# Kernel tuning notes

Measured on AMD Instinct MI355X. Metric: run time of the kernel, lower is better.

The kernel has to match this reference:

```python
import jax, jax.numpy as jnp
import numpy as np

B, S, D = 4, 2048, 1024
NUM_HEADS = 16
KQ = D // NUM_HEADS  # 64


def setup_inputs() -> dict:
    key = jax.random.key(0)
    ks = jax.random.split(key, 4)
    # he_uniform fan_in = D: limit = sqrt(6/fan_in)
    lim = np.sqrt(6.0 / D).astype(np.float32)
    x = jax.random.normal(ks[0], (B, S, D), dtype=jnp.float32)
    Wq = jax.random.uniform(ks[1], (D, KQ), minval=-lim, maxval=lim, dtype=jnp.float32)
    Wk = jax.random.uniform(ks[2], (D, KQ), minval=-lim, maxval=lim, dtype=jnp.float32)
    Wv = jax.random.uniform(ks[3], (D, KQ), minval=-lim, maxval=lim, dtype=jnp.float32)
    Bq = jnp.zeros((S, KQ), dtype=jnp.float32)
    Bk = jnp.zeros((S, KQ), dtype=jnp.float32)
    Bv = jnp.zeros((S, KQ), dtype=jnp.float32)
    return {"x": x, "Wq": Wq, "Bq": Bq, "Wk": Wk, "Bk": Bk, "Wv": Wv, "Bv": Bv}


def reference(x, Wq, Bq, Wk, Bk, Wv, Bv):
    # Q/K/V: [B,S,KQ]; biases are per-position [S,KQ], broadcast over batch
    Q = jnp.einsum('bsd,dk->bsk', x, Wq) + Bq
    K = jnp.einsum('bsd,dk->bsk', x, Wk) + Bk
    V = jnp.einsum('bsd,dk->bsk', x, Wv) + Bv
    scale = 1.0 / jnp.sqrt(jnp.float32(KQ))
    scores = jnp.einsum('bqk,bsk->bqs', Q, K) * scale  # [B,S,S]
    attn = jax.nn.softmax(scores, axis=-1)
    return jnp.einsum('bqs,bsk->bqk', attn, V)  # [B,S,KQ]
```

## Files before the change

kernel.cpp:

```cpp
#include <hip/hip_runtime.h>
#include <stdint.h>

#define NBATCH 4
#define NS 2048
#define ND 1024
#define NK 64
#define QSCALE 0.18033688011112042f

typedef __attribute__((ext_vector_type(4))) float f32x4;
typedef __attribute__((ext_vector_type(16))) float f32x16;
typedef __attribute__((ext_vector_type(8))) short bf16x8;
typedef unsigned short u16;
typedef unsigned int u32;
typedef unsigned long long u64;

__device__ __forceinline__ u16 f2bf(float f) {
  union { float f; u32 u; } v; v.f = f;
  u32 u = v.u;
  u += 0x7FFFu + ((u >> 16) & 1u);
  return (u16)(u >> 16);
}

__device__ __forceinline__ u32 pk2(float lo, float hi) {
  u32 r;
  asm("v_cvt_pk_bf16_f32 %0, %1, %2" : "=v"(r) : "v"(lo), "v"(hi));
  return r;
}

__global__ __launch_bounds__(256) void wtrans_kernel(
    const float* __restrict__ Wq, const float* __restrict__ Wk,
    const float* __restrict__ Wv, u16* __restrict__ Wt) {
  __shared__ float tile[64][65];
  int blk = blockIdx.x;
  int m = blk >> 4, dt = blk & 15;
  const float* W = (m == 0) ? Wq : (m == 1) ? Wk : Wv;
  int d0 = dt * 64;
  int t = threadIdx.x;
#pragma unroll
  for (int i = 0; i < 16; i++) {
    int idx = t + 256 * i;
    int dd = idx >> 6, c = idx & 63;
    tile[dd][c] = W[(d0 + dd) * 64 + c];
  }
  __syncthreads();
#pragma unroll
  for (int i = 0; i < 16; i++) {
    int idx = t + 256 * i;
    int c = idx >> 6, dd = idx & 63;
    Wt[(m * 64 + c) * 1024 + d0 + dd] = f2bf(tile[dd][c]);
  }
}

__global__ __launch_bounds__(512) void qkv_kernel(
    const float* __restrict__ x, const u16* __restrict__ Wt,
    const float* __restrict__ Bq, const float* __restrict__ Bk,
    const float* __restrict__ Bv, u16* __restrict__ Qf,
    u16* __restrict__ Kf, u16* __restrict__ Vf) {
  __shared__ __attribute__((aligned(16))) char lds[57344];
  char* ldsx = lds;
  char* ldsw = lds + 8192;

  int tid = threadIdx.x;
  int w = tid >> 6, lane = tid & 63;
  int g = lane >> 4, c = lane & 15;
  int rh = w & 1, cq = w >> 1;

  int xrow = tid >> 4;
  int xp4  = tid & 15;
  const float* xsrc = x + ((long)blockIdx.x * 32 + xrow) * ND + xp4 * 4;
  int xwoff = xrow * 128 + ((xp4 * 8) ^ ((xrow & 7) << 4));

  int wrow = tid >> 3;
  int wslot = tid & 7;
  const u16* wsrc0 = Wt + (long)wrow * ND + wslot * 8;
  const u16* wsrc1 = Wt + (long)(64 + wrow) * ND + wslot * 8;
  const u16* wsrc2 = Wt + (long)(128 + wrow) * ND + wslot * 8;
  int wswz = (wrow & 7) << 4;
  int wwoff0 = wrow * 128 + ((wslot * 16) ^ wswz);
  int wwoff1 = (64 + wrow) * 128 + ((wslot * 16) ^ wswz);
  int wwoff2 = (128 + wrow) * 128 + ((wslot * 16) ^ wswz);

  int rowa = rh * 16 + c;
  int aswz = (rowa & 7) << 4;
  int aoff0 = rowa * 128 + ((g * 16) ^ aswz);
  int aoff1 = rowa * 128 + ((64 + g * 16) ^ aswz);
  int boff00, boff01, boff10, boff11, boff20, boff21;
  {
    int col = cq * 48 + c;
    int bz = (col & 7) << 4;
    boff00 = col * 128 + ((g * 16) ^ bz);
    boff01 = col * 128 + ((64 + g * 16) ^ bz);
    col += 16; bz = (col & 7) << 4;
    boff10 = col * 128 + ((g * 16) ^ bz);
    boff11 = col * 128 + ((64 + g * 16) ^ bz);
    col += 16; bz = (col & 7) << 4;
    boff20 = col * 128 + ((g * 16) ^ bz);
    boff21 = col * 128 + ((64 + g * 16) ^ bz);
  }

  f32x4 acc[3];
#pragma unroll
  for (int tt = 0; tt < 3; tt++) acc[tt] = (f32x4){0.f, 0.f, 0.f, 0.f};

  f32x4 xst;
  bf16x8 wst0, wst1, wst2;

#define LOADS(T) do {                                   \
    xst  = *(const f32x4*)(xsrc + (T) * 64);            \
    wst0 = *(const bf16x8*)(wsrc0 + (T) * 64);          \
    wst1 = *(const bf16x8*)(wsrc1 + (T) * 64);          \
    wst2 = *(const bf16x8*)(wsrc2 + (T) * 64);          \
  } while (0)

#define WRITES(NB) do {                                 \
    u32 lo_ = pk2(xst[0], xst[1]);                      \
    u32 hi_ = pk2(xst[2], xst[3]);                      \
    *(u64*)(ldsx + (NB) * 4096 + xwoff) = ((u64)hi_ << 32) | lo_; \
    *(bf16x8*)(ldsw + (NB) * 24576 + wwoff0) = wst0;    \
    *(bf16x8*)(ldsw + (NB) * 24576 + wwoff1) = wst1;    \
    *(bf16x8*)(ldsw + (NB) * 24576 + wwoff2) = wst2;    \
  } while (0)

#define COMPUTE(B) do {                                 \
    const char* xb_ = ldsx + (B) * 4096;                \
    const char* wb_ = ldsw + (B) * 24576;               \
    bf16x8 a0_ = *(const bf16x8*)(xb_ + aoff0);         \
    bf16x8 a1_ = *(const bf16x8*)(xb_ + aoff1);         \
    acc[0] = __builtin_amdgcn_mfma_f32_16x16x32_bf16(a0_, *(const bf16x8*)(wb_ + boff00), acc[0], 0, 0, 0); \
    acc[0] = __builtin_amdgcn_mfma_f32_16x16x32_bf16(a1_, *(const bf16x8*)(wb_ + boff01), acc[0], 0, 0, 0); \
    acc[1] = __builtin_amdgcn_mfma_f32_16x16x32_bf16(a0_, *(const bf16x8*)(wb_ + boff10), acc[1], 0, 0, 0); \
    acc[1] = __builtin_amdgcn_mfma_f32_16x16x32_bf16(a1_, *(const bf16x8*)(wb_ + boff11), acc[1], 0, 0, 0); \
    acc[2] = __builtin_amdgcn_mfma_f32_16x16x32_bf16(a0_, *(const bf16x8*)(wb_ + boff20), acc[2], 0, 0, 0); \
    acc[2] = __builtin_amdgcn_mfma_f32_16x16x32_bf16(a1_, *(const bf16x8*)(wb_ + boff21), acc[2], 0, 0, 0); \
  } while (0)

  LOADS(0);
  WRITES(0);
  __syncthreads();
#pragma unroll
  for (int t = 0; t < 16; t++) {
    if (t < 15) LOADS(t + 1);
    __builtin_amdgcn_sched_barrier(0);
    COMPUTE(t & 1);
    if (t < 15) WRITES((t + 1) & 1);
    __syncthreads();
  }
#undef LOADS
#undef WRITES
#undef COMPUTE

  long r0 = (long)blockIdx.x * 32 + rh * 16 + 4 * g;
#pragma unroll
  for (int tt = 0; tt < 3; tt++) {
    int colg = cq * 48 + tt * 16 + c;
    int mtx = colg >> 6;
    int col = colg & 63;
    const float* Bias = (mtx == 0) ? Bq : (mtx == 1) ? Bk : Bv;
    u16* Out = (mtx == 0) ? Qf : (mtx == 1) ? Kf : Vf;
#pragma unroll
    for (int j = 0; j < 4; j++) {
      long r = r0 + j;
      int srow = (int)(r & (NS - 1));
      int bb = (int)(r >> 11);
      float v = acc[tt][j] + Bias[srow * NK + col];
      if (mtx == 0) v *= QSCALE;
      long addr;
      if (mtx < 2) {
        addr = (((long)bb * 64 + (srow >> 5)) * 4 + (col >> 4)) * 512
             + (long)((srow & 31) + ((col >> 3) & 1) * 32) * 8 + (col & 7);
      } else {
        addr = ((((long)bb * 2 + ((col >> 5) & 1)) * 32 + (srow >> 6)) * 4 + ((srow >> 4) & 3)) * 512
             + (long)((col & 31) + ((srow >> 3) & 1) * 32) * 8 + (srow & 7);
      }
      Out[addr] = f2bf(v);
    }
  }
}

__device__ __forceinline__ bf16x8 pack8(float p0, float p1, float p2, float p3,
                                        float p4, float p5, float p6, float p7,
                                        int hi) {
  u32 A = pk2(p0, p1), B = pk2(p2, p3), C = pk2(p4, p5), D = pk2(p6, p7);
  u32 sA = (u32)__shfl_xor((int)A, 32);
  u32 sB = (u32)__shfl_xor((int)B, 32);
  u32 sC = (u32)__shfl_xor((int)C, 32);
  u32 sD = (u32)__shfl_xor((int)D, 32);
  union { u32 w[4]; bf16x8 v; } u;
  u.w[0] = hi ? sC : A;
  u.w[1] = hi ? sD : B;
  u.w[2] = hi ? C : sA;
  u.w[3] = hi ? D : sB;
  return u.v;
}

__global__ __launch_bounds__(512) void attn_kernel(
    const u16* __restrict__ Qf, const u16* __restrict__ Kf,
    const u16* __restrict__ Vf, float* __restrict__ out) {
  __shared__ float Ol[8][32][64];
  __shared__ float Ll[8][32];
  int w = threadIdx.x >> 6, lane = threadIdx.x & 63;
  int q = lane & 31, hi = lane >> 5;
  int bid = blockIdx.x;
  int b = (bid & 7) >> 1;
  int qt = ((bid >> 3) << 1) | (bid & 1);
  long qglob = (long)b * NS + qt * 32;

  bf16x8 qf[4];
  {
    const u16* qp = Qf + ((long)b * 64 + qt) * 2048 + lane * 8;
#pragma unroll
    for (int kk = 0; kk < 4; kk++) qf[kk] = *(const bf16x8*)(qp + kk * 512);
  }
  const u16* kcp = Kf + ((long)b * 64 + w * 8) * 2048 + lane * 8;
  const u16* vcp0 = Vf + ((long)b * 64 + w * 4) * 2048 + lane * 8;
  const u16* vcp1 = Vf + ((long)(b * 2 + 1) * 32 + w * 4) * 2048 + lane * 8;

  f32x16 o0, o1;
#pragma unroll
  for (int r = 0; r < 16; r++) { o0[r] = 0.f; o1[r] = 0.f; }
  float lacc[4] = {0.f, 0.f, 0.f, 0.f};

  bf16x8 kA0[4], kA1[4], kB0[4], kB1[4];
#pragma unroll
  for (int kk = 0; kk < 4; kk++) {
    kA0[kk] = *(const bf16x8*)(kcp + kk * 512);
    kA1[kk] = *(const bf16x8*)(kcp + 2048 + kk * 512);
  }

#define ATTN_STEP(T, KC0, KC1, KN0, KN1)                                      \
  do {                                                                        \
    int t_ = (T);                                                             \
    bf16x8 vf0[4], vf1[4];                                                    \
    _Pragma("unroll") for (int i = 0; i < 4; i++) {                           \
      vf0[i] = *(const bf16x8*)(vcp0 + t_ * 2048 + i * 512);                  \
      vf1[i] = *(const bf16x8*)(vcp1 + t_ * 2048 + i * 512);                  \
    }                                                                         \
    if (t_ + 1 < 4) {                                                         \
      const u16* kn_ = kcp + (long)(t_ + 1) * 4096;                           \
      _Pragma("unroll") for (int i = 0; i < 4; i++) {                         \
        KN0[i] = *(const bf16x8*)(kn_ + i * 512);                             \
        KN1[i] = *(const bf16x8*)(kn_ + 2048 + i * 512);                      \
      }                                                                       \
    }                                                                         \
    __builtin_amdgcn_sched_barrier(0);                                        \
    f32x16 s0, s1;                                                            \
    _Pragma("unroll") for (int r = 0; r < 16; r++) { s0[r] = 0.f; s1[r] = 0.f; } \
    _Pragma("unroll") for (int i = 0; i < 4; i++)                             \
      s0 = __builtin_amdgcn_mfma_f32_32x32x16_bf16(KC0[i], qf[i], s0, 0, 0, 0); \
    _Pragma("unroll") for (int i = 0; i < 4; i++)                             \
      s1 = __builtin_amdgcn_mfma_f32_32x32x16_bf16(KC1[i], qf[i], s1, 0, 0, 0); \
    _Pragma("unroll") for (int r = 0; r < 16; r++) {                          \
      s0[r] = exp2f(s0[r]); s1[r] = exp2f(s1[r]);                             \
      lacc[r & 3] += s0[r] + s1[r];                                           \
    }                                                                         \
    bf16x8 pa[4];                                                             \
    pa[0] = pack8(s0[0], s0[1], s0[2], s0[3], s0[4], s0[5], s0[6], s0[7], hi);   \
    pa[1] = pack8(s0[8], s0[9], s0[10], s0[11], s0[12], s0[13], s0[14], s0[15], hi); \
    pa[2] = pack8(s1[0], s1[1], s1[2], s1[3], s1[4], s1[5], s1[6], s1[7], hi);   \
    pa[3] = pack8(s1[8], s1[9], s1[10], s1[11], s1[12], s1[13], s1[14], s1[15], hi); \
    _Pragma("unroll") for (int i = 0; i < 4; i++) {                           \
      o0 = __builtin_amdgcn_mfma_f32_32x32x16_bf16(pa[i], vf0[i], o0, 0, 0, 0); \
      o1 = __builtin_amdgcn_mfma_f32_32x32x16_bf16(pa[i], vf1[i], o1, 0, 0, 0); \
    }                                                                         \
  } while (0)

  ATTN_STEP(0, kA0, kA1, kB0, kB1);
  ATTN_STEP(1, kB0, kB1, kA0, kA1);
  ATTN_STEP(2, kA0, kA1, kB0, kB1);
  ATTN_STEP(3, kB0, kB1, kA0, kA1);
#undef ATTN_STEP

  float lt = (lacc[0] + lacc[1]) + (lacc[2] + lacc[3]);
  lt += __shfl_xor(lt, 32);

#pragma unroll
  for (int r = 0; r < 16; r++) {
    int qq = (r & 3) + 8 * (r >> 2) + 4 * hi;
    Ol[w][qq][q]      = o0[r];
    Ol[w][qq][q + 32] = o1[r];
  }
  if (hi == 0) Ll[w][q] = lt;
  __syncthreads();

#pragma unroll
  for (int rr = 4; rr >= 1; rr >>= 1) {
    if (w < rr) {
#pragma unroll
      for (int i = 0; i < 8; i++) {
        int idx = lane + i * 64;
        f32x4* dst = (f32x4*)&Ol[w][idx >> 4][(idx & 15) * 4];
        const f32x4* src = (const f32x4*)&Ol[w + rr][idx >> 4][(idx & 15) * 4];
        *dst += *src;
      }
      if (lane < 32) Ll[w][lane] += Ll[w + rr][lane];
    }
    __syncthreads();
  }

  {
    int idx = threadIdx.x;
    int row = idx >> 4, c4 = (idx & 15) * 4;
    float inv = 1.0f / Ll[0][row];
    f32x4 v = *(const f32x4*)&Ol[0][row][c4];
    f32x4 r;
#pragma unroll
    for (int i = 0; i < 4; i++) r[i] = v[i] * inv;
    *(f32x4*)&out[(qglob + row) * NK + c4] = r;
  }
}

extern "C" void kernel_launch(void* const* d_in, const int* in_sizes, int n_in,
                              void* d_out, int out_size, void* d_ws, size_t ws_size,
                              hipStream_t stream) {
  const float* x  = (const float*)d_in[0];
  const float* Wq = (const float*)d_in[1];
  const float* Bq = (const float*)d_in[2];
  const float* Wk = (const float*)d_in[3];
  const float* Bk = (const float*)d_in[4];
  const float* Wv = (const float*)d_in[5];
  const float* Bv = (const float*)d_in[6];
  float* out = (float*)d_out;

  char* ws = (char*)d_ws;
  u16* Wt = (u16*)ws;
  u16* Qf = (u16*)(ws + 393216);
  u16* Kf = (u16*)(ws + 1441792);
  u16* Vf = (u16*)(ws + 2490368);

  wtrans_kernel<<<dim3(48), dim3(256), 0, stream>>>(Wq, Wk, Wv, Wt);
  qkv_kernel<<<dim3(256), dim3(512), 0, stream>>>(x, Wt, Bq, Bk, Bv, Qf, Kf, Vf);
  attn_kernel<<<dim3(256), dim3(512), 0, stream>>>(Qf, Kf, Vf, out);
}
```

Measured before the change: 34.19 us.

## Share K/V tiles across waves via double-buffered LDS and split keys across blocks

```diff
diff --git a/kernel.cpp b/kernel.cpp
--- a/kernel.cpp
+++ b/kernel.cpp
@@ -193,62 +193,71 @@
   return u.v;
 }
 
-__global__ __launch_bounds__(512) void attn_kernel(
+__global__ __launch_bounds__(256) void attn_kernel(
     const u16* __restrict__ Qf, const u16* __restrict__ Kf,
-    const u16* __restrict__ Vf, float* __restrict__ out) {
-  __shared__ float Ol[8][32][64];
-  __shared__ float Ll[8][32];
-  int w = threadIdx.x >> 6, lane = threadIdx.x & 63;
+    const u16* __restrict__ Vf, float* __restrict__ Opart,
+    float* __restrict__ lpart) {
+  __shared__ __attribute__((aligned(16))) char kv[2][16384];
+  int tid = threadIdx.x;
+  int w = tid >> 6, lane = tid & 63;
   int q = lane & 31, hi = lane >> 5;
   int bid = blockIdx.x;
-  int b = (bid & 7) >> 1;
-  int qt = ((bid >> 3) << 1) | (bid & 1);
-  long qglob = (long)b * NS + qt * 32;
+  int xcd = bid & 7, i5 = bid >> 3;
+  int combo = xcd * 2 + (i5 & 1);
+  int qt4 = i5 >> 1;
+  int b = combo >> 2, sp = combo & 3;
 
   bf16x8 qf[4];
   {
-    const u16* qp = Qf + ((long)b * 64 + qt) * 2048 + lane * 8;
+    const u16* qp = Qf + ((long)b * 64 + qt4 * 4 + w) * 2048 + lane * 8;
 #pragma unroll
     for (int kk = 0; kk < 4; kk++) qf[kk] = *(const bf16x8*)(qp + kk * 512);
   }
-  const u16* kcp = Kf + ((long)b * 64 + w * 8) * 2048 + lane * 8;
-  const u16* vcp0 = Vf + ((long)b * 64 + w * 4) * 2048 + lane * 8;
-  const u16* vcp1 = Vf + ((long)(b * 2 + 1) * 32 + w * 4) * 2048 + lane * 8;
+
+  const char* ksrc = (const char*)(Kf + ((long)b * 64 + sp * 16) * 2048);
+  const char* v0src = (const char*)(Vf + ((long)(b * 2) * 32 + sp * 8) * 2048);
+  const char* v1src = (const char*)(Vf + ((long)(b * 2 + 1) * 32 + sp * 8) * 2048);
+  const char* src_base = (w == 0) ? ksrc : (w == 1) ? (ksrc + 4096)
+                       : (w == 2) ? v0src : v1src;
+  long src_step = (w < 2) ? 8192 : 4096;
+  int ldsoff = w * 4096 + lane * 16;
 
   f32x16 o0, o1;
 #pragma unroll
   for (int r = 0; r < 16; r++) { o0[r] = 0.f; o1[r] = 0.f; }
   float lacc[4] = {0.f, 0.f, 0.f, 0.f};
 
-  bf16x8 kA0[4], kA1[4], kB0[4], kB1[4];
-#pragma unroll
-  for (int kk = 0; kk < 4; kk++) {
-    kA0[kk] = *(const bf16x8*)(kcp + kk * 512);
-    kA1[kk] = *(const bf16x8*)(kcp + 2048 + kk * 512);
-  }
-
-#define ATTN_STEP(T, KC0, KC1, KN0, KN1)                                      \
-  do {                                                                        \
-    int t_ = (T);                                                             \
-    bf16x8 vf0[4], vf1[4];                                                    \
+  bf16x8 g0, g1, g2, g3;
+#define SLOAD(T) do {                                                   \
+    const char* s_ = src_base + (long)(T) * src_step + lane * 16;       \
+    g0 = *(const bf16x8*)(s_);                                          \
+    g1 = *(const bf16x8*)(s_ + 1024);                                   \
+    g2 = *(const bf16x8*)(s_ + 2048);                                   \
+    g3 = *(const bf16x8*)(s_ + 3072);                                   \
+  } while (0)
+#define SWRITE(NB) do {                                                 \
+    char* d_ = kv[NB] + ldsoff;                                         \
+    *(bf16x8*)(d_)        = g0;                                         \
+    *(bf16x8*)(d_ + 1024) = g1;                                         \
+    *(bf16x8*)(d_ + 2048) = g2;                                         \
+    *(bf16x8*)(d_ + 3072) = g3;                                         \
+  } while (0)
+
+#define ASTEP(T) do {                                                         \
+    const char* base_ = kv[(T) & 1];                                          \
+    bf16x8 kf0[4], kf1[4], vf0[4], vf1[4];                                    \
     _Pragma("unroll") for (int i = 0; i < 4; i++) {                           \
-      vf0[i] = *(const bf16x8*)(vcp0 + t_ * 2048 + i * 512);                  \
-      vf1[i] = *(const bf16x8*)(vcp1 + t_ * 2048 + i * 512);                  \
+      kf0[i] = *(const bf16x8*)(base_ + i * 1024 + lane * 16);                \
+      kf1[i] = *(const bf16x8*)(base_ + 4096 + i * 1024 + lane * 16);         \
+      vf0[i] = *(const bf16x8*)(base_ + 8192 + i * 1024 + lane * 16);         \
+      vf1[i] = *(const bf16x8*)(base_ + 12288 + i * 1024 + lane * 16);        \
     }                                                                         \
-    if (t_ + 1 < 4) {                                                         \
-      const u16* kn_ = kcp + (long)(t_ + 1) * 4096;                           \
-      _Pragma("unroll") for (int i = 0; i < 4; i++) {                         \
-        KN0[i] = *(const bf16x8*)(kn_ + i * 512);                             \
-        KN1[i] = *(const bf16x8*)(kn_ + 2048 + i * 512);                      \
-      }                                                                       \
-    }                                                                         \
-    __builtin_amdgcn_sched_barrier(0);                                        \
     f32x16 s0, s1;                                                            \
     _Pragma("unroll") for (int r = 0; r < 16; r++) { s0[r] = 0.f; s1[r] = 0.f; } \
     _Pragma("unroll") for (int i = 0; i < 4; i++)                             \
-      s0 = __builtin_amdgcn_mfma_f32_32x32x16_bf16(KC0[i], qf[i], s0, 0, 0, 0); \
+      s0 = __builtin_amdgcn_mfma_f32_32x32x16_bf16(kf0[i], qf[i], s0, 0, 0, 0); \
     _Pragma("unroll") for (int i = 0; i < 4; i++)                             \
-      s1 = __builtin_amdgcn_mfma_f32_32x32x16_bf16(KC1[i], qf[i], s1, 0, 0, 0); \
+      s1 = __builtin_amdgcn_mfma_f32_32x32x16_bf16(kf1[i], qf[i], s1, 0, 0, 0); \
     _Pragma("unroll") for (int r = 0; r < 16; r++) {                          \
       s0[r] = exp2f(s0[r]); s1[r] = exp2f(s1[r]);                             \
       lacc[r & 3] += s0[r] + s1[r];                                           \
@@ -264,49 +273,51 @@
     }                                                                         \
   } while (0)
 
-  ATTN_STEP(0, kA0, kA1, kB0, kB1);
-  ATTN_STEP(1, kB0, kB1, kA0, kA1);
-  ATTN_STEP(2, kA0, kA1, kB0, kB1);
-  ATTN_STEP(3, kB0, kB1, kA0, kA1);
-#undef ATTN_STEP
+  SLOAD(0);
+  SWRITE(0);
+  __syncthreads();
+#pragma unroll
+  for (int t = 0; t < 8; t++) {
+    if (t < 7) SLOAD(t + 1);
+    ASTEP(t);
+    if (t < 7) SWRITE((t + 1) & 1);
+    __syncthreads();
+  }
+#undef SLOAD
+#undef SWRITE
+#undef ASTEP
 
   float lt = (lacc[0] + lacc[1]) + (lacc[2] + lacc[3]);
   lt += __shfl_xor(lt, 32);
 
+  long qbase = (long)b * NS + (qt4 * 4 + w) * 32;
+  long ob = (long)sp * (NBATCH * NS * NK);
 #pragma unroll
   for (int r = 0; r < 16; r++) {
     int qq = (r & 3) + 8 * (r >> 2) + 4 * hi;
-    Ol[w][qq][q]      = o0[r];
-    Ol[w][qq][q + 32] = o1[r];
-  }
-  if (hi == 0) Ll[w][q] = lt;
-  __syncthreads();
-
-#pragma unroll
-  for (int rr = 4; rr >= 1; rr >>= 1) {
-    if (w < rr) {
-#pragma unroll
-      for (int i = 0; i < 8; i++) {
-        int idx = lane + i * 64;
-        f32x4* dst = (f32x4*)&Ol[w][idx >> 4][(idx & 15) * 4];
-        const f32x4* src = (const f32x4*)&Ol[w + rr][idx >> 4][(idx & 15) * 4];
-        *dst += *src;
-      }
-      if (lane < 32) Ll[w][lane] += Ll[w + rr][lane];
-    }
-    __syncthreads();
-  }
-
-  {
-    int idx = threadIdx.x;
-    int row = idx >> 4, c4 = (idx & 15) * 4;
-    float inv = 1.0f / Ll[0][row];
-    f32x4 v = *(const f32x4*)&Ol[0][row][c4];
-    f32x4 r;
-#pragma unroll
-    for (int i = 0; i < 4; i++) r[i] = v[i] * inv;
-    *(f32x4*)&out[(qglob + row) * NK + c4] = r;
-  }
+    float* op = Opart + ob + (qbase + qq) * NK + q;
+    op[0]  = o0[r];
+    op[32] = o1[r];
+  }
+  if (hi == 0) lpart[sp * (NBATCH * NS) + qbase + q] = lt;
+}
+
+__global__ __launch_bounds__(256) void combine_kernel(
+    const float* __restrict__ Opart, const float* __restrict__ lpart,
+    float* __restrict__ out, int nsplit) {
+  int gid = blockIdx.x * 256 + threadIdx.x;
+  int rw = gid >> 4, c4 = (gid & 15) * 4;
+  f32x4 a = (f32x4){0.f, 0.f, 0.f, 0.f};
+  float l = 0.f;
+  for (int sp = 0; sp < nsplit; sp++) {
+    a += *(const f32x4*)(Opart + (long)sp * (NBATCH * NS * NK) + (long)rw * NK + c4);
+    l += lpart[sp * (NBATCH * NS) + rw];
+  }
+  float inv = 1.0f / l;
+  f32x4 r;
+#pragma unroll
+  for (int i = 0; i < 4; i++) r[i] = a[i] * inv;
+  *(f32x4*)(out + (long)rw * NK + c4) = r;
 }
 
 extern "C" void kernel_launch(void* const* d_in, const int* in_sizes, int n_in,
@@ -326,8 +337,11 @@
   u16* Qf = (u16*)(ws + 393216);
   u16* Kf = (u16*)(ws + 1441792);
   u16* Vf = (u16*)(ws + 2490368);
+  float* lpart = (float*)(ws + 3538944);
+  float* Opart = (float*)(ws + 3801088);
 
   wtrans_kernel<<<dim3(48), dim3(256), 0, stream>>>(Wq, Wk, Wv, Wt);
   qkv_kernel<<<dim3(256), dim3(512), 0, stream>>>(x, Wt, Bq, Bk, Bv, Qf, Kf, Vf);
-  attn_kernel<<<dim3(256), dim3(512), 0, stream>>>(Qf, Kf, Vf, out);
-}
+  attn_kernel<<<dim3(256), dim3(256), 0, stream>>>(Qf, Kf, Vf, Opart, lpart);
+  combine_kernel<<<dim3(512), dim3(256), 0, stream>>>(Opart, lpart, out, 4);
+}
```

Result: slower. 40.18 us (+17.5%).

## Use direct global-to-LDS loads with triple buffering and staged epilogue stores in QKV

Applied to the files above, without the earlier changes.

```diff
diff --git a/kernel.cpp b/kernel.cpp
--- a/kernel.cpp
+++ b/kernel.cpp
@@ -25,6 +25,12 @@
   u32 r;
   asm("v_cvt_pk_bf16_f32 %0, %1, %2" : "=v"(r) : "v"(lo), "v"(hi));
   return r;
+}
+
+__device__ __forceinline__ void gll16(const void* g, void* l) {
+  __builtin_amdgcn_global_load_lds(
+      (const __attribute__((address_space(1))) unsigned int*)g,
+      (__attribute__((address_space(3))) unsigned int*)l, 16, 0, 0);
 }
 
 __global__ __launch_bounds__(256) void wtrans_kernel(
@@ -56,124 +62,125 @@
     const float* __restrict__ Bq, const float* __restrict__ Bk,
     const float* __restrict__ Bv, u16* __restrict__ Qf,
     u16* __restrict__ Kf, u16* __restrict__ Vf) {
-  __shared__ __attribute__((aligned(16))) char lds[57344];
+  __shared__ __attribute__((aligned(16))) char lds[98304];
   char* ldsx = lds;
-  char* ldsw = lds + 8192;
+  char* ldsw = lds + 24576;
 
   int tid = threadIdx.x;
   int w = tid >> 6, lane = tid & 63;
   int g = lane >> 4, c = lane & 15;
   int rh = w & 1, cq = w >> 1;
 
-  int xrow = tid >> 4;
-  int xp4  = tid & 15;
-  const float* xsrc = x + ((long)blockIdx.x * 32 + xrow) * ND + xp4 * 4;
-  int xwoff = xrow * 128 + ((xp4 * 8) ^ ((xrow & 7) << 4));
-
-  int wrow = tid >> 3;
-  int wslot = tid & 7;
-  const u16* wsrc0 = Wt + (long)wrow * ND + wslot * 8;
-  const u16* wsrc1 = Wt + (long)(64 + wrow) * ND + wslot * 8;
-  const u16* wsrc2 = Wt + (long)(128 + wrow) * ND + wslot * 8;
-  int wswz = (wrow & 7) << 4;
-  int wwoff0 = wrow * 128 + ((wslot * 16) ^ wswz);
-  int wwoff1 = (64 + wrow) * 128 + ((wslot * 16) ^ wswz);
-  int wwoff2 = (128 + wrow) * 128 + ((wslot * 16) ^ wswz);
+  int xrow_l = 4 * w + (lane >> 4);
+  long xrow_g = (long)blockIdx.x * 32 + xrow_l;
+  int xs32 = ((lane >> 1) & 7) ^ (xrow_l & 7);
+  const char* xg = (const char*)(x + xrow_g * ND) + xs32 * 32 + (lane & 1) * 16;
+
+  int wr0 = 8 * w + (lane >> 3);
+  const char* wg0 = (const char*)(Wt + (long)(wr0)       * ND) + (((lane & 7) ^ (wr0 & 7)) * 16);
+  const char* wg1 = (const char*)(Wt + (long)(64 + wr0)  * ND) + (((lane & 7) ^ (wr0 & 7)) * 16);
+  const char* wg2 = (const char*)(Wt + (long)(128 + wr0) * ND) + (((lane & 7) ^ (wr0 & 7)) * 16);
+  int wd0 = (8 * w) * 128, wd1 = (64 + 8 * w) * 128, wd2 = (128 + 8 * w) * 128;
 
   int rowa = rh * 16 + c;
-  int aswz = (rowa & 7) << 4;
-  int aoff0 = rowa * 128 + ((g * 16) ^ aswz);
-  int aoff1 = rowa * 128 + ((64 + g * 16) ^ aswz);
-  int boff00, boff01, boff10, boff11, boff20, boff21;
-  {
-    int col = cq * 48 + c;
-    int bz = (col & 7) << 4;
-    boff00 = col * 128 + ((g * 16) ^ bz);
-    boff01 = col * 128 + ((64 + g * 16) ^ bz);
-    col += 16; bz = (col & 7) << 4;
-    boff10 = col * 128 + ((g * 16) ^ bz);
-    boff11 = col * 128 + ((64 + g * 16) ^ bz);
-    col += 16; bz = (col & 7) << 4;
-    boff20 = col * 128 + ((g * 16) ^ bz);
-    boff21 = col * 128 + ((64 + g * 16) ^ bz);
+  int axor = rowa & 7;
+  int aoff0 = rowa * 256 + ((g ^ axor) * 32);
+  int aoff1 = rowa * 256 + (((4 + g) ^ axor) * 32);
+  int boff[3][2];
+#pragma unroll
+  for (int tt = 0; tt < 3; tt++) {
+    int col = cq * 48 + tt * 16 + c;
+#pragma unroll
+    for (int kk = 0; kk < 2; kk++)
+      boff[tt][kk] = col * 128 + (((kk * 4 + g) ^ (col & 7)) * 16);
   }
 
   f32x4 acc[3];
 #pragma unroll
   for (int tt = 0; tt < 3; tt++) acc[tt] = (f32x4){0.f, 0.f, 0.f, 0.f};
 
-  f32x4 xst;
-  bf16x8 wst0, wst1, wst2;
-
-#define LOADS(T) do {                                   \
-    xst  = *(const f32x4*)(xsrc + (T) * 64);            \
-    wst0 = *(const bf16x8*)(wsrc0 + (T) * 64);          \
-    wst1 = *(const bf16x8*)(wsrc1 + (T) * 64);          \
-    wst2 = *(const bf16x8*)(wsrc2 + (T) * 64);          \
+#define STAGE(BUF, T) do {                                            \
+    gll16(xg + (long)(T) * 256, ldsx + (BUF) * 8192 + w * 1024);      \
+    gll16(wg0 + (T) * 128, ldsw + (BUF) * 24576 + wd0);               \
+    gll16(wg1 + (T) * 128, ldsw + (BUF) * 24576 + wd1);               \
+    gll16(wg2 + (T) * 128, ldsw + (BUF) * 24576 + wd2);               \
   } while (0)
 
-#define WRITES(NB) do {                                 \
-    u32 lo_ = pk2(xst[0], xst[1]);                      \
-    u32 hi_ = pk2(xst[2], xst[3]);                      \
-    *(u64*)(ldsx + (NB) * 4096 + xwoff) = ((u64)hi_ << 32) | lo_; \
-    *(bf16x8*)(ldsw + (NB) * 24576 + wwoff0) = wst0;    \
-    *(bf16x8*)(ldsw + (NB) * 24576 + wwoff1) = wst1;    \
-    *(bf16x8*)(ldsw + (NB) * 24576 + wwoff2) = wst2;    \
+#define COMPUTE(B) do {                                               \
+    const char* xb_ = ldsx + (B) * 8192;                              \
+    const char* wb_ = ldsw + (B) * 24576;                             \
+    f32x4 p0_ = *(const f32x4*)(xb_ + aoff0);                         \
+    f32x4 p1_ = *(const f32x4*)(xb_ + aoff0 + 16);                    \
+    f32x4 p2_ = *(const f32x4*)(xb_ + aoff1);                         \
+    f32x4 p3_ = *(const f32x4*)(xb_ + aoff1 + 16);                    \
+    union { bf16x8 v; u32 w[4]; } af0, af1;                           \
+    af0.w[0] = pk2(p0_[0], p0_[1]); af0.w[1] = pk2(p0_[2], p0_[3]);   \
+    af0.w[2] = pk2(p1_[0], p1_[1]); af0.w[3] = pk2(p1_[2], p1_[3]);   \
+    af1.w[0] = pk2(p2_[0], p2_[1]); af1.w[1] = pk2(p2_[2], p2_[3]);   \
+    af1.w[2] = pk2(p3_[0], p3_[1]); af1.w[3] = pk2(p3_[2], p3_[3]);   \
+    _Pragma("unroll")                                                 \
+    for (int tt = 0; tt < 3; tt++) {                                  \
+      bf16x8 b0_ = *(const bf16x8*)(wb_ + boff[tt][0]);               \
+      bf16x8 b1_ = *(const bf16x8*)(wb_ + boff[tt][1]);               \
+      acc[tt] = __builtin_amdgcn_mfma_f32_16x16x32_bf16(af0.v, b0_, acc[tt], 0, 0, 0); \
+      acc[tt] = __builtin_amdgcn_mfma_f32_16x16x32_bf16(af1.v, b1_, acc[tt], 0, 0, 0); \
+    }                                                                 \
   } while (0)
 
-#define COMPUTE(B) do {                                 \
-    const char* xb_ = ldsx + (B) * 4096;                \
-    const char* wb_ = ldsw + (B) * 24576;               \
-    bf16x8 a0_ = *(const bf16x8*)(xb_ + aoff0);         \
-    bf16x8 a1_ = *(const bf16x8*)(xb_ + aoff1);         \
-    acc[0] = __builtin_amdgcn_mfma_f32_16x16x32_bf16(a0_, *(const bf16x8*)(wb_ + boff00), acc[0], 0, 0, 0); \
-    acc[0] = __builtin_amdgcn_mfma_f32_16x16x32_bf16(a1_, *(const bf16x8*)(wb_ + boff01), acc[0], 0, 0, 0); \
-    acc[1] = __builtin_amdgcn_mfma_f32_16x16x32_bf16(a0_, *(const bf16x8*)(wb_ + boff10), acc[1], 0, 0, 0); \
-    acc[1] = __builtin_amdgcn_mfma_f32_16x16x32_bf16(a1_, *(const bf16x8*)(wb_ + boff11), acc[1], 0, 0, 0); \
-    acc[2] = __builtin_amdgcn_mfma_f32_16x16x32_bf16(a0_, *(const bf16x8*)(wb_ + boff20), acc[2], 0, 0, 0); \
-    acc[2] = __builtin_amdgcn_mfma_f32_16x16x32_bf16(a1_, *(const bf16x8*)(wb_ + boff21), acc[2], 0, 0, 0); \
-  } while (0)
-
-  LOADS(0);
-  WRITES(0);
+  STAGE(0, 0);
+  STAGE(1, 1);
+#pragma unroll
+  for (int t = 0; t < 16; t++) {
+    if (t < 15) asm volatile("s_waitcnt vmcnt(4)" ::: "memory");
+    else        asm volatile("s_waitcnt vmcnt(0)" ::: "memory");
+    __builtin_amdgcn_s_barrier();
+    __builtin_amdgcn_sched_barrier(0);
+    if (t + 2 < 16) STAGE((t + 2) % 3, t + 2);
+    __builtin_amdgcn_sched_barrier(0);
+    COMPUTE(t % 3);
+  }
+#undef STAGE
+#undef COMPUTE
+
   __syncthreads();
-#pragma unroll
-  for (int t = 0; t < 16; t++) {
-    if (t < 15) LOADS(t + 1);
-    __builtin_amdgcn_sched_barrier(0);
-    COMPUTE(t & 1);
-    if (t < 15) WRITES((t + 1) & 1);
-    __syncthreads();
-  }
-#undef LOADS
-#undef WRITES
-#undef COMPUTE
-
-  long r0 = (long)blockIdx.x * 32 + rh * 16 + 4 * g;
+  u16* ep = (u16*)lds;
+  int il = blockIdx.x & 63, bb = blockIdx.x >> 6;
 #pragma unroll
   for (int tt = 0; tt < 3; tt++) {
     int colg = cq * 48 + tt * 16 + c;
     int mtx = colg >> 6;
     int col = colg & 63;
     const float* Bias = (mtx == 0) ? Bq : (mtx == 1) ? Bk : Bv;
-    u16* Out = (mtx == 0) ? Qf : (mtx == 1) ? Kf : Vf;
 #pragma unroll
     for (int j = 0; j < 4; j++) {
-      long r = r0 + j;
-      int srow = (int)(r & (NS - 1));
-      int bb = (int)(r >> 11);
-      float v = acc[tt][j] + Bias[srow * NK + col];
+      int sl = rh * 16 + 4 * g + j;
+      float v = acc[tt][j] + Bias[(il * 32 + sl) * NK + col];
       if (mtx == 0) v *= QSCALE;
-      long addr;
+      int chunk, off;
       if (mtx < 2) {
-        addr = (((long)bb * 64 + (srow >> 5)) * 4 + (col >> 4)) * 512
-             + (long)((srow & 31) + ((col >> 3) & 1) * 32) * 8 + (col & 7);
+        chunk = mtx * 4 + (col >> 4);
+        off = (sl + ((col >> 3) & 1) * 32) * 8 + (col & 7);
       } else {
-        addr = ((((long)bb * 2 + ((col >> 5) & 1)) * 32 + (srow >> 6)) * 4 + ((srow >> 4) & 3)) * 512
-             + (long)((col & 31) + ((srow >> 3) & 1) * 32) * 8 + (srow & 7);
+        chunk = 8 + (col >> 5) * 2 + (sl >> 4);
+        off = ((col & 31) + ((sl >> 3) & 1) * 32) * 8 + (sl & 7);
       }
-      Out[addr] = f2bf(v);
+      ep[chunk * 512 + off] = f2bf(v);
     }
+  }
+  __syncthreads();
+  for (int t5 = tid; t5 < 768; t5 += 512) {
+    int ch = t5 >> 6, pc = t5 & 63;
+    bf16x8 val = *(const bf16x8*)(ep + ch * 512 + pc * 8);
+    u16* dst;
+    if (ch < 4)
+      dst = Qf + (((long)bb * 64 + il) * 4 + ch) * 512 + pc * 8;
+    else if (ch < 8)
+      dst = Kf + (((long)bb * 64 + il) * 4 + (ch - 4)) * 512 + pc * 8;
+    else {
+      int half = (ch - 8) >> 1, iv = (ch - 8) & 1;
+      dst = Vf + ((((long)bb * 2 + half) * 32 + (il >> 1)) * 4 + 2 * (il & 1) + iv) * 512 + pc * 8;
+    }
+    *(bf16x8*)dst = val;
   }
 }
 
```

Measured after the change: 31.57 us. -7.7%, faster.
